# Kernel optimization log

Hardware: AMD Instinct MI355X
Metric: run time of the kernel (lower is better)

## Reference

```python
import jax, jax.numpy as jnp
import numpy as np
import math

INPUT_DIM = 256
HIDDEN_DIM = 128
N = 8192
GATE_TEMPERATURE = 1.0
LN_EPS = 1e-5


def setup_inputs() -> dict:
    key = jax.random.key(0)
    ks = jax.random.split(key, 10)
    s_in = 1.0 / math.sqrt(INPUT_DIM)
    s_h = 1.0 / math.sqrt(HIDDEN_DIM)
    s_cat = 1.0 / math.sqrt(INPUT_DIM + HIDDEN_DIM)
    return {
        "node_features": jax.random.normal(ks[0], (N, INPUT_DIM), jnp.float32),
        "adj_matrix": jax.random.uniform(ks[1], (N, N), jnp.float32),
        "msg_w": jax.random.uniform(ks[2], (INPUT_DIM, HIDDEN_DIM), jnp.float32, -s_in, s_in),
        "msg_b": jax.random.uniform(ks[3], (HIDDEN_DIM,), jnp.float32, -s_in, s_in),
        "upd_w": jax.random.uniform(ks[4], (INPUT_DIM + HIDDEN_DIM, HIDDEN_DIM), jnp.float32, -s_cat, s_cat),
        "upd_b": jax.random.uniform(ks[5], (HIDDEN_DIM,), jnp.float32, -s_cat, s_cat),
        "gate_q_w": jax.random.uniform(ks[6], (HIDDEN_DIM, HIDDEN_DIM), jnp.float32, -s_h, s_h),
        "gate_k_w": jax.random.uniform(ks[7], (HIDDEN_DIM, HIDDEN_DIM), jnp.float32, -s_h, s_h),
        "gate_bias": jnp.float32(-1.0),
        "ln_gamma": jnp.ones((HIDDEN_DIM,), jnp.float32),
        "ln_beta": jnp.zeros((HIDDEN_DIM,), jnp.float32),
    }


def reference(node_features, adj_matrix, msg_w, msg_b, upd_w, upd_b,
              gate_q_w, gate_k_w, gate_bias, ln_gamma, ln_beta):
    # messages: [N, hidden]
    messages = node_features @ msg_w + msg_b
    # edge gates: sigmoid(QK^T / (sqrt(d)*tau) + b), masked by adjacency
    q = messages @ gate_q_w  # [N, hidden]
    k = messages @ gate_k_w  # [N, hidden]
    scale = 1.0 / (math.sqrt(HIDDEN_DIM) * max(GATE_TEMPERATURE, 1e-6))
    scores = (q @ k.T) * scale  # [N, N]
    gates_masked = jax.nn.sigmoid(scores + gate_bias) * adj_matrix
    aggregated = gates_masked @ messages  # [N, hidden]
    combined = jnp.concatenate([node_features, aggregated], axis=1)
    updated = jax.nn.relu(combined @ upd_w + upd_b)
    # LayerNorm over last dim
    mu = jnp.mean(updated, axis=-1, keepdims=True)
    var = jnp.var(updated, axis=-1, keepdims=True)
    normed = (updated - mu) * jax.lax.rsqrt(var + LN_EPS)
    return normed * ln_gamma + ln_beta
```

## Files before the change

### kernel.cpp

```cpp
#include <hip/hip_runtime.h>
#include <hip/hip_bf16.h>
#include <stdint.h>

#define NN 8192
#define DIN 256
#define HID 128
#define SCALE 0.08838834764831845f

typedef __attribute__((ext_vector_type(8))) short short8;
typedef __attribute__((ext_vector_type(4))) float f32x4;
typedef __attribute__((ext_vector_type(16))) float f32x16;
typedef __attribute__((ext_vector_type(8))) unsigned short u16x8;
typedef __attribute__((ext_vector_type(4))) unsigned int u32x4;

__device__ __forceinline__ unsigned short f2bf(float f) {
  unsigned int u = __builtin_bit_cast(unsigned int, f);
  u += 0x7FFFu + ((u >> 16) & 1u);
  return (unsigned short)(u >> 16);
}

__device__ __forceinline__ unsigned int cvtpk(float lo, float hi) {
  unsigned int r;
  asm("v_cvt_pk_bf16_f32 %0, %1, %2" : "=v"(r) : "v"(lo), "v"(hi));
  return r;
}

__device__ __forceinline__ void async16(const void* g, void* l) {
  __builtin_amdgcn_global_load_lds(
      (const __attribute__((address_space(1))) unsigned int*)g,
      (__attribute__((address_space(3))) unsigned int*)l, 16, 0, 0);
}

__global__ __launch_bounds__(256) void kw0(
    const float* __restrict__ msg_w, const float* __restrict__ qw,
    const float* __restrict__ kw, const float* __restrict__ upd_w,
    unsigned short* __restrict__ mwT, unsigned short* __restrict__ qwT,
    unsigned short* __restrict__ kwT, unsigned short* __restrict__ w_t) {
  int idx0 = blockIdx.x * 1792 + threadIdx.x;
#pragma unroll
  for (int it = 0; it < 7; ++it) {
    int idx = idx0 + it * 256;
    if (idx < 32768) {
      int h = idx >> 8, j = idx & 255;
      mwT[idx] = f2bf(msg_w[j * HID + h]);
    } else if (idx < 49152) {
      int r = idx - 32768, h = r >> 7, j = r & 127;
      qwT[r] = f2bf(qw[j * HID + h]);
    } else if (idx < 65536) {
      int r = idx - 49152, h = r >> 7, j = r & 127;
      kwT[r] = f2bf(kw[j * HID + h]);
    } else {
      int r = idx - 65536, h = r / 384, j = r % 384;
      w_t[r] = f2bf(upd_w[j * HID + h]);
    }
  }
}

__global__ __launch_bounds__(256) void ka(
    const float* __restrict__ nf, const unsigned short* __restrict__ mwT,
    const float* __restrict__ msg_b, const unsigned short* __restrict__ qwT,
    const unsigned short* __restrict__ kwT, unsigned short* __restrict__ q_bf,
    unsigned short* __restrict__ k_bf, unsigned short* __restrict__ m_t,
    unsigned short* __restrict__ nf_bf) {
  __shared__ __align__(16) unsigned short nfl[32][264];
  __shared__ __align__(16) unsigned short ml[32][136];
  int t = threadIdx.x, l = t & 63, w = t >> 6;
  int lr = l & 15, lg = l >> 4;
  int i0 = blockIdx.x * 32;
  {
    int row = t >> 3, c0 = (t & 7) * 32;
    const float* src = nf + (size_t)(i0 + row) * DIN + c0;
    unsigned short* gdst = nf_bf + (size_t)(i0 + row) * DIN + c0;
#pragma unroll
    for (int v = 0; v < 4; ++v) {
      f32x4 a = *(const f32x4*)(src + v * 8);
      f32x4 b = *(const f32x4*)(src + v * 8 + 4);
      u16x8 o;
#pragma unroll
      for (int e = 0; e < 4; ++e) { o[e] = f2bf(a[e]); o[4 + e] = f2bf(b[e]); }
      *(u16x8*)&nfl[row][c0 + v * 8] = o;
      *(u16x8*)(gdst + v * 8) = o;
    }
  }
  __syncthreads();
  int rl = (w >> 1) * 16;
  int nb = (w & 1) * 4;
  f32x4 macc[4];
#pragma unroll
  for (int nt = 0; nt < 4; ++nt) macc[nt] = (f32x4){0.f, 0.f, 0.f, 0.f};
#pragma unroll
  for (int kk = 0; kk < 8; ++kk) {
    short8 af = *(const short8*)&nfl[rl + lr][kk * 32 + lg * 8];
#pragma unroll
    for (int nt = 0; nt < 4; ++nt) {
      short8 bf = *(const short8*)(mwT + (size_t)((nb + nt) * 16 + lr) * DIN + kk * 32 + lg * 8);
      macc[nt] = __builtin_amdgcn_mfma_f32_16x16x32_bf16(af, bf, macc[nt], 0, 0, 0);
    }
  }
#pragma unroll
  for (int nt = 0; nt < 4; ++nt) {
    int col = (nb + nt) * 16 + lr;
    float bias = msg_b[col];
#pragma unroll
    for (int reg = 0; reg < 4; ++reg)
      ml[rl + lg * 4 + reg][col] = f2bf(macc[nt][reg] + bias);
  }
  __syncthreads();
  {
    int hh = t >> 1;
    int Ibase = (t & 1) * 16;
    int I = i0 + Ibase;
    unsigned short* mb =
        m_t + ((size_t)(I >> 4) * 4 + (hh >> 5)) * 512 + (hh & 31) * 8;
    u16x8 o0, o1;
#pragma unroll
    for (int v = 0; v < 8; ++v) {
      o0[v] = ml[Ibase + v][hh];
      o1[v] = ml[Ibase + 8 + v][hh];
    }
    *(u16x8*)(mb) = o0;
    *(u16x8*)(mb + 256) = o1;
  }
  f32x4 qacc[4], kacc[4];
#pragma unroll
  for (int nt = 0; nt < 4; ++nt) {
    qacc[nt] = (f32x4){0.f, 0.f, 0.f, 0.f};
    kacc[nt] = (f32x4){0.f, 0.f, 0.f, 0.f};
  }
#pragma unroll
  for (int kk = 0; kk < 4; ++kk) {
    short8 af = *(const short8*)&ml[rl + lr][kk * 32 + lg * 8];
#pragma unroll
    for (int nt = 0; nt < 4; ++nt) {
      short8 bq = *(const short8*)(qwT + (size_t)((nb + nt) * 16 + lr) * HID + kk * 32 + lg * 8);
      short8 bk = *(const short8*)(kwT + (size_t)((nb + nt) * 16 + lr) * HID + kk * 32 + lg * 8);
      qacc[nt] = __builtin_amdgcn_mfma_f32_16x16x32_bf16(af, bq, qacc[nt], 0, 0, 0);
      kacc[nt] = __builtin_amdgcn_mfma_f32_16x16x32_bf16(af, bk, kacc[nt], 0, 0, 0);
    }
  }
#pragma unroll
  for (int nt = 0; nt < 4; ++nt) {
    int col = (nb + nt) * 16 + lr;
#pragma unroll
    for (int reg = 0; reg < 4; ++reg) {
      int row = i0 + rl + lg * 4 + reg;
      q_bf[(size_t)row * HID + col] = f2bf(qacc[nt][reg]);
      size_t ko = ((size_t)(row >> 5) * 8 + (col >> 4)) * 512 +
                  (((col >> 3) & 1) * 32 + (row & 31)) * 8 + (col & 7);
      k_bf[ko] = f2bf(kacc[nt][reg]);
    }
  }
}

__global__ __launch_bounds__(256, 3) void kb(
    const unsigned short* __restrict__ q_bf, const unsigned short* __restrict__ k_bf,
    const unsigned short* __restrict__ m_t, const float* __restrict__ adj,
    const float* __restrict__ gate_bias, float* __restrict__ agg_parts) {
  __shared__ __align__(16) char klds[16384];
  __shared__ __align__(16) char mlds[16384];
  int t = threadIdx.x, l = t & 63, w = t >> 6;
  int li = l & 31, hi = l >> 5;
  int lin = blockIdx.x + blockIdx.y * 64;
  int nlin = (lin & 7) * 128 + (lin >> 3);
  int bx = nlin & 63, by = nlin >> 6;
  int i0 = bx * 128;
  int jbase = by * 512;
  float gb = gate_bias[0];

  int irow = i0 + w * 32 + li;
  short8 qf[8];
#pragma unroll
  for (int kc16 = 0; kc16 < 8; ++kc16)
    qf[kc16] = *(const short8*)(q_bf + (size_t)irow * HID + kc16 * 16 + hi * 8);

  const float* arow = adj + (size_t)irow * NN;

  const char* kread = klds + l * 16;
  const char* mread = mlds + l * 16;

  f32x16 acc[4];
#pragma unroll
  for (int ht = 0; ht < 4; ++ht)
#pragma unroll
    for (int r = 0; r < 16; ++r) acc[ht][r] = 0.f;

  for (int jt = 0; jt < 8; ++jt) {
    int j0 = jbase + jt * 64;
    __syncthreads();
    f32x4 adjv[8];
#pragma unroll
    for (int q2 = 0; q2 < 8; ++q2)
      adjv[q2] = *(const f32x4*)(arow + j0 + (q2 >> 2) * 32 + (q2 & 3) * 8 + hi * 4);
    {
      const unsigned short* ksrc = k_bf + (size_t)j0 * 128;
      const unsigned short* msrc = m_t + (size_t)j0 * 128;
#pragma unroll
      for (int p = 0; p < 4; ++p)
        async16(ksrc + p * 2048 + t * 8, klds + p * 4096 + w * 1024);
#pragma unroll
      for (int p = 0; p < 4; ++p)
        async16(msrc + p * 2048 + t * 8, mlds + p * 4096 + w * 1024);
    }
    __syncthreads();

#pragma unroll
    for (int jt32 = 0; jt32 < 2; ++jt32) {
      f32x16 s;
#pragma unroll
      for (int r = 0; r < 16; ++r) s[r] = 0.f;
#pragma unroll
      for (int kc16 = 0; kc16 < 8; ++kc16) {
        const short8 kf = *(const short8*)(kread + jt32 * 8192 + kc16 * 1024);
        s = __builtin_amdgcn_mfma_f32_32x32x16_bf16(kf, qf[kc16], s, 0, 0, 0);
      }
      float g[16];
#pragma unroll
      for (int r = 0; r < 16; ++r) {
        float x = fmaf(s[r], SCALE, gb);
        float e = __expf(-x);
        g[r] = adjv[jt32 * 4 + (r >> 2)][r & 3] * __builtin_amdgcn_rcpf(1.0f + e);
      }
#pragma unroll
      for (int kc = 0; kc < 2; ++kc) {
        unsigned int r0 = cvtpk(g[kc * 8 + 0], g[kc * 8 + 1]);
        unsigned int r1 = cvtpk(g[kc * 8 + 2], g[kc * 8 + 3]);
        unsigned int r2 = cvtpk(g[kc * 8 + 4], g[kc * 8 + 5]);
        unsigned int r3 = cvtpk(g[kc * 8 + 6], g[kc * 8 + 7]);
        asm volatile("v_permlane32_swap_b32 %0, %1" : "+v"(r0), "+v"(r2));
        asm volatile("v_permlane32_swap_b32 %0, %1" : "+v"(r1), "+v"(r3));
        const short8 gf = __builtin_bit_cast(short8, (u32x4){r0, r1, r2, r3});
        int jblk = (jt32 * 2 + kc) * 4096;
#pragma unroll
        for (int ht = 0; ht < 4; ++ht) {
          const short8 mf = *(const short8*)(mread + jblk + ht * 1024);
          acc[ht] = __builtin_amdgcn_mfma_f32_32x32x16_bf16(mf, gf, acc[ht], 0, 0, 0);
        }
      }
    }
  }
  float* part = agg_parts + (size_t)by * HID * NN;
#pragma unroll
  for (int ht = 0; ht < 4; ++ht)
#pragma unroll
    for (int r = 0; r < 16; ++r) {
      int h = ht * 32 + (r & 3) + 8 * (r >> 2) + 4 * hi;
      part[(size_t)h * NN + i0 + w * 32 + li] = acc[ht][r];
    }
}

__global__ __launch_bounds__(256) void kc(
    const unsigned short* __restrict__ nf_bf, const float* __restrict__ agg_parts,
    const unsigned short* __restrict__ w_t, const float* __restrict__ upd_b,
    const float* __restrict__ gamma, const float* __restrict__ beta,
    float* __restrict__ out) {
  __shared__ __align__(16) unsigned short aggl[64][136];
  int t = threadIdx.x, l = t & 63, w = t >> 6;
  int i0 = blockIdx.x * 64;
  {
    const size_t ps = (size_t)HID * NN;
#pragma unroll
    for (int pass = 0; pass < 8; ++pass) {
      int h = pass * 16 + (t >> 4);
      const float* pb = agg_parts + (size_t)h * NN + i0 + (t & 15) * 4;
      f32x4 s = (f32x4){0.f, 0.f, 0.f, 0.f};
#pragma unroll
      for (int c = 0; c < 16; ++c) s += *(const f32x4*)(pb + c * ps);
#pragma unroll
      for (int e = 0; e < 4; ++e) aggl[(t & 15) * 4 + e][h] = f2bf(s[e]);
    }
  }
  __syncthreads();
  int lr = l & 15, lg = l >> 4;
  int arow = i0 + w * 16 + lr;
  short8 af[12];
#pragma unroll
  for (int kk = 0; kk < 8; ++kk)
    af[kk] = *(const short8*)(nf_bf + (size_t)arow * DIN + kk * 32 + lg * 8);
#pragma unroll
  for (int kk = 8; kk < 12; ++kk)
    af[kk] = *(const short8*)(&aggl[w * 16 + lr][(kk - 8) * 32 + lg * 8]);
  f32x4 acc[8];
#pragma unroll
  for (int nt = 0; nt < 8; ++nt) acc[nt] = (f32x4){0.f, 0.f, 0.f, 0.f};
#pragma unroll
  for (int kk = 0; kk < 12; ++kk)
#pragma unroll
    for (int nt = 0; nt < 8; ++nt) {
      const short8 bf =
          *(const short8*)(w_t + (size_t)(nt * 16 + lr) * 384 + kk * 32 + lg * 8);
      acc[nt] = __builtin_amdgcn_mfma_f32_16x16x32_bf16(af[kk], bf, acc[nt], 0, 0, 0);
    }
  float ub[8], ga[8], be[8];
#pragma unroll
  for (int nt = 0; nt < 8; ++nt) {
    ub[nt] = upd_b[nt * 16 + lr];
    ga[nt] = gamma[nt * 16 + lr];
    be[nt] = beta[nt * 16 + lr];
  }
  float v[8][4], sum[4], sq[4];
#pragma unroll
  for (int reg = 0; reg < 4; ++reg) { sum[reg] = 0.f; sq[reg] = 0.f; }
#pragma unroll
  for (int nt = 0; nt < 8; ++nt)
#pragma unroll
    for (int reg = 0; reg < 4; ++reg) {
      float x = acc[nt][reg] + ub[nt];
      x = fmaxf(x, 0.f);
      v[nt][reg] = x;
      sum[reg] += x;
      sq[reg] = fmaf(x, x, sq[reg]);
    }
#pragma unroll
  for (int reg = 0; reg < 4; ++reg) {
#pragma unroll
    for (int m = 1; m < 16; m <<= 1) {
      sum[reg] += __shfl_xor(sum[reg], m, 16);
      sq[reg] += __shfl_xor(sq[reg], m, 16);
    }
  }
#pragma unroll
  for (int reg = 0; reg < 4; ++reg) {
    float mu = sum[reg] * (1.0f / 128.0f);
    float var = sq[reg] * (1.0f / 128.0f) - mu * mu;
    float rstd = rsqrtf(var + 1e-5f);
    int orow = i0 + w * 16 + lg * 4 + reg;
#pragma unroll
    for (int nt = 0; nt < 8; ++nt) {
      float y = (v[nt][reg] - mu) * rstd * ga[nt] + be[nt];
      out[(size_t)orow * HID + nt * 16 + lr] = y;
    }
  }
}

extern "C" void kernel_launch(void* const* d_in, const int* in_sizes, int n_in,
                              void* d_out, int out_size, void* d_ws, size_t ws_size,
                              hipStream_t stream) {
  const float* nf    = (const float*)d_in[0];
  const float* adj   = (const float*)d_in[1];
  const float* msg_w = (const float*)d_in[2];
  const float* msg_b = (const float*)d_in[3];
  const float* upd_w = (const float*)d_in[4];
  const float* upd_b = (const float*)d_in[5];
  const float* qw    = (const float*)d_in[6];
  const float* kw    = (const float*)d_in[7];
  const float* gbias = (const float*)d_in[8];
  const float* gamma = (const float*)d_in[9];
  const float* beta  = (const float*)d_in[10];
  char* ws = (char*)d_ws;
  unsigned short* q_bf  = (unsigned short*)(ws);
  unsigned short* k_bf  = (unsigned short*)(ws + 0x200000);
  unsigned short* m_t   = (unsigned short*)(ws + 0x400000);
  unsigned short* nf_bf = (unsigned short*)(ws + 0x600000);
  unsigned short* w_t   = (unsigned short*)(ws + 0xA00000);
  unsigned short* mwT   = (unsigned short*)(ws + 0xA20000);
  unsigned short* qwT   = (unsigned short*)(ws + 0xA30000);
  unsigned short* kwT   = (unsigned short*)(ws + 0xA38000);
  float* agg            = (float*)(ws + 0xA40000);

  kw0<<<64, 256, 0, stream>>>(msg_w, qw, kw, upd_w, mwT, qwT, kwT, w_t);
  ka<<<256, 256, 0, stream>>>(nf, mwT, msg_b, qwT, kwT, q_bf, k_bf, m_t, nf_bf);
  kb<<<dim3(64, 16), 256, 0, stream>>>(q_bf, k_bf, m_t, adj, gbias, agg);
  kc<<<128, 256, 0, stream>>>(nf_bf, agg, w_t, upd_b, gamma, beta, (float*)d_out);
}
```

Baseline: 135.2 us.

## Double-buffer K/M LDS tiles and adjacency loads in gated aggregation kernel

The main aggregation kernel now keeps two LDS buffers each for K and messages and two register sets for adjacency values. It issues the async copies and adjacency loads for the next 64-column tile before computing the current one, with one barrier per tile instead of two. This is meant to overlap global-to-LDS traffic and the HBM reads of the adjacency matrix with the MFMA and sigmoid work. LDS use doubles to 64KB per block and extra registers are held, so the occupancy hint drops from 3 to 2 blocks per CU. The last iteration prefetches a wrapped-around tile that is never used, which adds some wasted traffic.

Result: slower. 138.5 us (+2.5%).

```diff
diff --git a/kernel.cpp b/kernel.cpp
--- a/kernel.cpp
+++ b/kernel.cpp
@@ -152,12 +152,63 @@
   }
 }
 
-__global__ __launch_bounds__(256, 3) void kb(
+#define LOADADJ(dst, j0v)                                                     \
+  {                                                                           \
+    _Pragma("unroll") for (int q2 = 0; q2 < 8; ++q2)                          \
+        dst[q2] = *(const f32x4*)(arow + (j0v) + (q2 >> 2) * 32 +             \
+                                  (q2 & 3) * 8 + hi * 4);                     \
+  }
+
+#define STAGE(bufi, j0v)                                                      \
+  {                                                                           \
+    const unsigned short* ksrc = k_bf + (size_t)(j0v) * 128;                  \
+    const unsigned short* msrc = m_t + (size_t)(j0v) * 128;                   \
+    _Pragma("unroll") for (int p = 0; p < 4; ++p)                             \
+        async16(ksrc + p * 2048 + t * 8, &klds[bufi][p * 4096 + w * 1024]);   \
+    _Pragma("unroll") for (int p = 0; p < 4; ++p)                             \
+        async16(msrc + p * 2048 + t * 8, &mlds[bufi][p * 4096 + w * 1024]);   \
+  }
+
+#define COMPUTE(bufi, adjv)                                                   \
+  _Pragma("unroll") for (int jt32 = 0; jt32 < 2; ++jt32) {                    \
+    f32x16 s;                                                                 \
+    _Pragma("unroll") for (int r = 0; r < 16; ++r) s[r] = 0.f;                \
+    _Pragma("unroll") for (int kc16 = 0; kc16 < 8; ++kc16) {                  \
+      const short8 kf = *(const short8*)(&klds[bufi][l * 16 + jt32 * 8192 +   \
+                                                     kc16 * 1024]);           \
+      s = __builtin_amdgcn_mfma_f32_32x32x16_bf16(kf, qf[kc16], s, 0, 0, 0);  \
+    }                                                                         \
+    float g[16];                                                              \
+    _Pragma("unroll") for (int r = 0; r < 16; ++r) {                          \
+      float x = fmaf(s[r], SCALE, gb);                                        \
+      float e = __expf(-x);                                                   \
+      g[r] = adjv[jt32 * 4 + (r >> 2)][r & 3] *                               \
+             __builtin_amdgcn_rcpf(1.0f + e);                                 \
+    }                                                                         \
+    _Pragma("unroll") for (int kc = 0; kc < 2; ++kc) {                        \
+      unsigned int r0 = cvtpk(g[kc * 8 + 0], g[kc * 8 + 1]);                  \
+      unsigned int r1 = cvtpk(g[kc * 8 + 2], g[kc * 8 + 3]);                  \
+      unsigned int r2 = cvtpk(g[kc * 8 + 4], g[kc * 8 + 5]);                  \
+      unsigned int r3 = cvtpk(g[kc * 8 + 6], g[kc * 8 + 7]);                  \
+      asm volatile("v_permlane32_swap_b32 %0, %1" : "+v"(r0), "+v"(r2));      \
+      asm volatile("v_permlane32_swap_b32 %0, %1" : "+v"(r1), "+v"(r3));      \
+      const short8 gf = __builtin_bit_cast(short8, (u32x4){r0, r1, r2, r3});  \
+      int jblk = (jt32 * 2 + kc) * 4096;                                      \
+      _Pragma("unroll") for (int ht = 0; ht < 4; ++ht) {                      \
+        const short8 mf = *(const short8*)(&mlds[bufi][l * 16 + jblk +        \
+                                                       ht * 1024]);           \
+        acc[ht] = __builtin_amdgcn_mfma_f32_32x32x16_bf16(mf, gf, acc[ht],    \
+                                                          0, 0, 0);           \
+      }                                                                       \
+    }                                                                         \
+  }
+
+__global__ __launch_bounds__(256, 2) void kb(
     const unsigned short* __restrict__ q_bf, const unsigned short* __restrict__ k_bf,
     const unsigned short* __restrict__ m_t, const float* __restrict__ adj,
     const float* __restrict__ gate_bias, float* __restrict__ agg_parts) {
-  __shared__ __align__(16) char klds[16384];
-  __shared__ __align__(16) char mlds[16384];
+  __shared__ __align__(16) char klds[2][16384];
+  __shared__ __align__(16) char mlds[2][16384];
   int t = threadIdx.x, l = t & 63, w = t >> 6;
   int li = l & 31, hi = l >> 5;
   int lin = blockIdx.x + blockIdx.y * 64;
@@ -175,68 +226,29 @@
 
   const float* arow = adj + (size_t)irow * NN;
 
-  const char* kread = klds + l * 16;
-  const char* mread = mlds + l * 16;
-
   f32x16 acc[4];
 #pragma unroll
   for (int ht = 0; ht < 4; ++ht)
 #pragma unroll
     for (int r = 0; r < 16; ++r) acc[ht][r] = 0.f;
 
-  for (int jt = 0; jt < 8; ++jt) {
-    int j0 = jbase + jt * 64;
+  f32x4 adjA[8], adjB[8];
+  STAGE(0, jbase);
+  LOADADJ(adjA, jbase);
+  __syncthreads();
+
+  for (int jp = 0; jp < 4; ++jp) {
+    int jt0 = jp * 2;
+    int j1 = jbase + ((jt0 + 1) & 7) * 64;
+    int j2 = jbase + ((jt0 + 2) & 7) * 64;
+    STAGE(1, j1);
+    LOADADJ(adjB, j1);
+    COMPUTE(0, adjA);
     __syncthreads();
-    f32x4 adjv[8];
-#pragma unroll
-    for (int q2 = 0; q2 < 8; ++q2)
-      adjv[q2] = *(const f32x4*)(arow + j0 + (q2 >> 2) * 32 + (q2 & 3) * 8 + hi * 4);
-    {
-      const unsigned short* ksrc = k_bf + (size_t)j0 * 128;
-      const unsigned short* msrc = m_t + (size_t)j0 * 128;
-#pragma unroll
-      for (int p = 0; p < 4; ++p)
-        async16(ksrc + p * 2048 + t * 8, klds + p * 4096 + w * 1024);
-#pragma unroll
-      for (int p = 0; p < 4; ++p)
-        async16(msrc + p * 2048 + t * 8, mlds + p * 4096 + w * 1024);
-    }
+    STAGE(0, j2);
+    LOADADJ(adjA, j2);
+    COMPUTE(1, adjB);
     __syncthreads();
-
-#pragma unroll
-    for (int jt32 = 0; jt32 < 2; ++jt32) {
-      f32x16 s;
-#pragma unroll
-      for (int r = 0; r < 16; ++r) s[r] = 0.f;
-#pragma unroll
-      for (int kc16 = 0; kc16 < 8; ++kc16) {
-        const short8 kf = *(const short8*)(kread + jt32 * 8192 + kc16 * 1024);
-        s = __builtin_amdgcn_mfma_f32_32x32x16_bf16(kf, qf[kc16], s, 0, 0, 0);
-      }
-      float g[16];
-#pragma unroll
-      for (int r = 0; r < 16; ++r) {
-        float x = fmaf(s[r], SCALE, gb);
-        float e = __expf(-x);
-        g[r] = adjv[jt32 * 4 + (r >> 2)][r & 3] * __builtin_amdgcn_rcpf(1.0f + e);
-      }
-#pragma unroll
-      for (int kc = 0; kc < 2; ++kc) {
-        unsigned int r0 = cvtpk(g[kc * 8 + 0], g[kc * 8 + 1]);
-        unsigned int r1 = cvtpk(g[kc * 8 + 2], g[kc * 8 + 3]);
-        unsigned int r2 = cvtpk(g[kc * 8 + 4], g[kc * 8 + 5]);
-        unsigned int r3 = cvtpk(g[kc * 8 + 6], g[kc * 8 + 7]);
-        asm volatile("v_permlane32_swap_b32 %0, %1" : "+v"(r0), "+v"(r2));
-        asm volatile("v_permlane32_swap_b32 %0, %1" : "+v"(r1), "+v"(r3));
-        const short8 gf = __builtin_bit_cast(short8, (u32x4){r0, r1, r2, r3});
-        int jblk = (jt32 * 2 + kc) * 4096;
-#pragma unroll
-        for (int ht = 0; ht < 4; ++ht) {
-          const short8 mf = *(const short8*)(mread + jblk + ht * 1024);
-          acc[ht] = __builtin_amdgcn_mfma_f32_32x32x16_bf16(mf, gf, acc[ht], 0, 0, 0);
-        }
-      }
-    }
   }
   float* part = agg_parts + (size_t)by * HID * NN;
 #pragma unroll
```

## Stage adjacency tiles through LDS with async loads and halve j-tile size

Applied to the files above, without the earlier changes.

Adjacency values are no longer read per thread straight from global memory into registers. They are now copied into a swizzled LDS buffer with async global-to-LDS loads, alongside the K and message tiles. The j-tile shrinks from 64 to 32 columns, so there are twice as many iterations and syncs, but the K/M LDS buffers are smaller and register pressure drops (no adjv[8] array). The aim is more coalesced, asynchronous adjacency streaming, since adjacency dominates memory traffic; the cost is more barriers per block and no prefetch overlap across iterations.

Result: slower. 138.6 us (+2.5%).

```diff
diff --git a/kernel.cpp b/kernel.cpp
--- a/kernel.cpp
+++ b/kernel.cpp
@@ -156,8 +156,9 @@
     const unsigned short* __restrict__ q_bf, const unsigned short* __restrict__ k_bf,
     const unsigned short* __restrict__ m_t, const float* __restrict__ adj,
     const float* __restrict__ gate_bias, float* __restrict__ agg_parts) {
-  __shared__ __align__(16) char klds[16384];
-  __shared__ __align__(16) char mlds[16384];
+  __shared__ __align__(16) char klds[8192];
+  __shared__ __align__(16) char mlds[8192];
+  __shared__ __align__(16) char alds[16384];
   int t = threadIdx.x, l = t & 63, w = t >> 6;
   int li = l & 31, hi = l >> 5;
   int lin = blockIdx.x + blockIdx.y * 64;
@@ -173,10 +174,12 @@
   for (int kc16 = 0; kc16 < 8; ++kc16)
     qf[kc16] = *(const short8*)(q_bf + (size_t)irow * HID + kc16 * 16 + hi * 8);
 
-  const float* arow = adj + (size_t)irow * NN;
-
   const char* kread = klds + l * 16;
   const char* mread = mlds + l * 16;
+  const char* aread = alds + (w * 32 + li) * 128;
+
+  int sarow = t >> 3;
+  int sachk = (t & 7) ^ (sarow & 7);
 
   f32x16 acc[4];
 #pragma unroll
@@ -184,57 +187,58 @@
 #pragma unroll
     for (int r = 0; r < 16; ++r) acc[ht][r] = 0.f;
 
-  for (int jt = 0; jt < 8; ++jt) {
-    int j0 = jbase + jt * 64;
+  for (int jt = 0; jt < 16; ++jt) {
+    int j0 = jbase + jt * 32;
     __syncthreads();
-    f32x4 adjv[8];
-#pragma unroll
-    for (int q2 = 0; q2 < 8; ++q2)
-      adjv[q2] = *(const f32x4*)(arow + j0 + (q2 >> 2) * 32 + (q2 & 3) * 8 + hi * 4);
     {
       const unsigned short* ksrc = k_bf + (size_t)j0 * 128;
       const unsigned short* msrc = m_t + (size_t)j0 * 128;
 #pragma unroll
-      for (int p = 0; p < 4; ++p)
+      for (int p = 0; p < 2; ++p)
         async16(ksrc + p * 2048 + t * 8, klds + p * 4096 + w * 1024);
 #pragma unroll
-      for (int p = 0; p < 4; ++p)
+      for (int p = 0; p < 2; ++p)
         async16(msrc + p * 2048 + t * 8, mlds + p * 4096 + w * 1024);
     }
+#pragma unroll
+    for (int p = 0; p < 4; ++p)
+      async16(adj + (size_t)(i0 + p * 32 + sarow) * NN + j0 + sachk * 4,
+              alds + p * 4096 + w * 1024);
     __syncthreads();
 
-#pragma unroll
-    for (int jt32 = 0; jt32 < 2; ++jt32) {
-      f32x16 s;
-#pragma unroll
-      for (int r = 0; r < 16; ++r) s[r] = 0.f;
-#pragma unroll
-      for (int kc16 = 0; kc16 < 8; ++kc16) {
-        const short8 kf = *(const short8*)(kread + jt32 * 8192 + kc16 * 1024);
-        s = __builtin_amdgcn_mfma_f32_32x32x16_bf16(kf, qf[kc16], s, 0, 0, 0);
+    f32x16 s;
+#pragma unroll
+    for (int r = 0; r < 16; ++r) s[r] = 0.f;
+#pragma unroll
+    for (int kc16 = 0; kc16 < 8; ++kc16) {
+      const short8 kf = *(const short8*)(kread + kc16 * 1024);
+      s = __builtin_amdgcn_mfma_f32_32x32x16_bf16(kf, qf[kc16], s, 0, 0, 0);
+    }
+#pragma unroll
+    for (int q = 0; q < 4; ++q) {
+      const f32x4 av =
+          *(const f32x4*)(aread + (((2 * q + hi) ^ (li & 7)) * 16));
+#pragma unroll
+      for (int e = 0; e < 4; ++e) {
+        int r = q * 4 + e;
+        float x = fmaf(s[r], SCALE, gb);
+        float ex = __expf(-x);
+        s[r] = av[e] * __builtin_amdgcn_rcpf(1.0f + ex);
       }
-      float g[16];
-#pragma unroll
-      for (int r = 0; r < 16; ++r) {
-        float x = fmaf(s[r], SCALE, gb);
-        float e = __expf(-x);
-        g[r] = adjv[jt32 * 4 + (r >> 2)][r & 3] * __builtin_amdgcn_rcpf(1.0f + e);
-      }
-#pragma unroll
-      for (int kc = 0; kc < 2; ++kc) {
-        unsigned int r0 = cvtpk(g[kc * 8 + 0], g[kc * 8 + 1]);
-        unsigned int r1 = cvtpk(g[kc * 8 + 2], g[kc * 8 + 3]);
-        unsigned int r2 = cvtpk(g[kc * 8 + 4], g[kc * 8 + 5]);
-        unsigned int r3 = cvtpk(g[kc * 8 + 6], g[kc * 8 + 7]);
-        asm volatile("v_permlane32_swap_b32 %0, %1" : "+v"(r0), "+v"(r2));
-        asm volatile("v_permlane32_swap_b32 %0, %1" : "+v"(r1), "+v"(r3));
-        const short8 gf = __builtin_bit_cast(short8, (u32x4){r0, r1, r2, r3});
-        int jblk = (jt32 * 2 + kc) * 4096;
-#pragma unroll
-        for (int ht = 0; ht < 4; ++ht) {
-          const short8 mf = *(const short8*)(mread + jblk + ht * 1024);
-          acc[ht] = __builtin_amdgcn_mfma_f32_32x32x16_bf16(mf, gf, acc[ht], 0, 0, 0);
-        }
+    }
+#pragma unroll
+    for (int kc = 0; kc < 2; ++kc) {
+      unsigned int r0 = cvtpk(s[kc * 8 + 0], s[kc * 8 + 1]);
+      unsigned int r1 = cvtpk(s[kc * 8 + 2], s[kc * 8 + 3]);
+      unsigned int r2 = cvtpk(s[kc * 8 + 4], s[kc * 8 + 5]);
+      unsigned int r3 = cvtpk(s[kc * 8 + 6], s[kc * 8 + 7]);
+      asm volatile("v_permlane32_swap_b32 %0, %1" : "+v"(r0), "+v"(r2));
+      asm volatile("v_permlane32_swap_b32 %0, %1" : "+v"(r1), "+v"(r3));
+      const short8 gf = __builtin_bit_cast(short8, (u32x4){r0, r1, r2, r3});
+#pragma unroll
+      for (int ht = 0; ht < 4; ++ht) {
+        const short8 mf = *(const short8*)(mread + kc * 4096 + ht * 1024);
+        acc[ht] = __builtin_amdgcn_mfma_f32_32x32x16_bf16(mf, gf, acc[ht], 0, 0, 0);
       }
     }
   }
```
